# Optimization experiments

Measured on AMD Instinct MI355X. Metric: run time of the kernel, lower is better.

The kernel has to match this reference:

```python
import jax, jax.numpy as jnp
import numpy as np

TOPK = 4


def setup_inputs() -> dict:
    key = jax.random.key(0)
    ks = jax.random.split(key, 9)
    B, T, D = 4, 2048, 1024
    E, H = 32, 128          # routed experts, per-expert hidden
    HS = H * TOPK           # shared expert hidden = 512
    s = lambda k, shape, fan: jax.random.normal(k, shape, dtype=jnp.float32) / np.sqrt(fan)
    return {
        "x": jax.random.normal(ks[0], (B, T, D), dtype=jnp.float32),
        "router_w": s(ks[1], (E, D), D),
        "router_bias": jnp.zeros((E,), dtype=jnp.float32),
        "gate_w": s(ks[2], (E, H, D), D),
        "up_w": s(ks[3], (E, H, D), D),
        "down_w": s(ks[4], (E, D, H), H),
        "sgate_w": s(ks[5], (HS, D), D),
        "sup_w": s(ks[6], (HS, D), D),
        "sdown_w": s(ks[7], (D, HS), HS),
    }


def reference(x, router_w, router_bias, gate_w, up_w, down_w, sgate_w, sup_w, sdown_w):
    B, T, D = x.shape
    flat = x.reshape(B * T, D)                                   # [N, D]
    # Router (fp32 logits + persistent bias buffer)
    logits = flat.astype(jnp.float32) @ router_w.T + router_bias  # [N, E]
    scores = jax.nn.softmax(logits, axis=-1)
    topk_scores, topk_idx = jax.lax.top_k(scores, TOPK)          # [N, K]
    topk_scores = topk_scores / jnp.clip(
        topk_scores.sum(axis=-1, keepdims=True), 1e-12, None)
    # Dense all-expert SwiGLU (matches torch.stack over experts)
    h = jax.nn.silu(jnp.einsum("nd,ehd->neh", flat, gate_w)) \
        * jnp.einsum("nd,ehd->neh", flat, up_w)                  # [N, E, H]
    expert_out = jnp.einsum("neh,edh->ned", h, down_w)           # [N, E, D]
    # Gather top-k expert outputs, scale, combine
    sel = jnp.take_along_axis(expert_out, topk_idx[:, :, None], axis=1)  # [N, K, D]
    out = (sel * topk_scores.astype(flat.dtype)[:, :, None]).sum(axis=1)  # [N, D]
    # Always-on shared expert (SwiGLU)
    out = out + (jax.nn.silu(flat @ sgate_w.T) * (flat @ sup_w.T)) @ sdown_w.T
    return out.reshape(B, T, D)
```

## Files before the change

kernel.cpp:

```cpp
#include <hip/hip_runtime.h>
#include <hip/hip_bf16.h>
#include <math.h>

#define N_TOK 8192
#define DIM   1024
#define E_R   32
#define H_E   128
#define HS    512
#define TOPK  4
#define RKS   8
#define RKL   (DIM / RKS)
#define MAXSLOT 34816

typedef __bf16 bf16;
typedef __bf16 bf16x8 __attribute__((ext_vector_type(8)));
typedef float  floatx4 __attribute__((ext_vector_type(4)));

#define MFMA16(a,b,c) __builtin_amdgcn_mfma_f32_16x16x32_bf16(a,b,c,0,0,0)

__device__ __forceinline__ void gl_lds16(const bf16* g, bf16* l) {
    __builtin_amdgcn_global_load_lds(
        (const __attribute__((address_space(1))) void*)g,
        (__attribute__((address_space(3))) void*)l, 16, 0, 0);
}

__device__ __forceinline__ int xcd_swz(int b, int n) {
    int q = n >> 3, r = n & 7;
    int xcd = b & 7, idx = b >> 3;
    return (xcd < r ? xcd * (q + 1) : r * (q + 1) + (xcd - r) * q) + idx;
}

__global__ __launch_bounds__(256)
void cvt_all(const float* __restrict__ x, const float* __restrict__ g,
             const float* __restrict__ u, const float* __restrict__ d,
             const float* __restrict__ sg, const float* __restrict__ su,
             const float* __restrict__ sd,
             bf16* __restrict__ xb, bf16* __restrict__ gb, bf16* __restrict__ ub,
             bf16* __restrict__ db, bf16* __restrict__ sgb, bf16* __restrict__ sub,
             bf16* __restrict__ sdb) {
    int b = blockIdx.x;
    const float* s; bf16* o; int lb;
    if      (b < 4096)  { s = x;  o = xb;  lb = b; }
    else if (b < 6144)  { s = g;  o = gb;  lb = b - 4096; }
    else if (b < 8192)  { s = u;  o = ub;  lb = b - 6144; }
    else if (b < 10240) { s = d;  o = db;  lb = b - 8192; }
    else if (b < 10496) { s = sg; o = sgb; lb = b - 10240; }
    else if (b < 10752) { s = su; o = sub; lb = b - 10496; }
    else                { s = sd; o = sdb; lb = b - 10752; }
    size_t i = (size_t)lb * 2048 + threadIdx.x * 8;
    float4 v0 = *(const float4*)(s + i);
    float4 v1 = *(const float4*)(s + i + 4);
    bf16x8 r = {(bf16)v0.x,(bf16)v0.y,(bf16)v0.z,(bf16)v0.w,
                (bf16)v1.x,(bf16)v1.y,(bf16)v1.z,(bf16)v1.w};
    *(bf16x8*)(o + i) = r;
}

__global__ __launch_bounds__(256)
void router_gemm(const float* __restrict__ x, const float* __restrict__ rw,
                 float* __restrict__ partial) {
    __shared__ float Xs[64 * 132];
    __shared__ float Wt[128 * 32];
    int tid = threadIdx.x;
    int t0  = blockIdx.x * 64;
    int kb  = blockIdx.y * RKL;

#pragma unroll
    for (int j = 0; j < 8; ++j) {
        int flat = j * 1024 + tid * 4;
        int row = flat >> 7, col = flat & 127;
        float4 v = *(const float4*)(x + (size_t)(t0 + row) * DIM + kb + col);
        *(float4*)(&Xs[row * 132 + col]) = v;
    }
    {
        int e = tid >> 3, kq = (tid & 7) * 16;
        const float* wp = rw + (size_t)e * DIM + kb + kq;
#pragma unroll
        for (int i = 0; i < 16; i += 4) {
            float4 v = *(const float4*)(wp + i);
            Wt[(kq + i + 0) * 32 + e] = v.x;
            Wt[(kq + i + 1) * 32 + e] = v.y;
            Wt[(kq + i + 2) * 32 + e] = v.z;
            Wt[(kq + i + 3) * 32 + e] = v.w;
        }
    }
    __syncthreads();

    int eg = tid & 7, tg = tid >> 3;
    float acc[2][4] = {{0.f}};
#pragma unroll 4
    for (int k = 0; k < RKL; k += 4) {
        float4 xa0 = *(const float4*)(&Xs[(tg * 2 + 0) * 132 + k]);
        float4 xa1 = *(const float4*)(&Xs[(tg * 2 + 1) * 132 + k]);
#pragma unroll
        for (int kk = 0; kk < 4; ++kk) {
            float4 w = *(const float4*)(&Wt[(k + kk) * 32 + eg * 4]);
            float x0 = (&xa0.x)[kk], x1 = (&xa1.x)[kk];
            acc[0][0] += x0 * w.x; acc[0][1] += x0 * w.y;
            acc[0][2] += x0 * w.z; acc[0][3] += x0 * w.w;
            acc[1][0] += x1 * w.x; acc[1][1] += x1 * w.y;
            acc[1][2] += x1 * w.z; acc[1][3] += x1 * w.w;
        }
    }
#pragma unroll
    for (int t = 0; t < 2; ++t) {
        floatx4 v = { acc[t][0], acc[t][1], acc[t][2], acc[t][3] };
        *(floatx4*)(&partial[((size_t)blockIdx.y * N_TOK + t0 + tg * 2 + t) * 32 + eg * 4]) = v;
    }
}

__global__ __launch_bounds__(256)
void router_fin(const float* __restrict__ partial, const float* __restrict__ rb,
                int* __restrict__ counts, int* __restrict__ tlist,
                float* __restrict__ slist, int* __restrict__ tok2slot) {
    __shared__ int lcnt[E_R];
    __shared__ int gbase[E_R];
    int tid = threadIdx.x;
    int n = blockIdx.x * 256 + tid;
    if (tid < E_R) lcnt[tid] = 0;
    __syncthreads();

    float lg[E_R];
#pragma unroll
    for (int e4 = 0; e4 < E_R; e4 += 4) {
        floatx4 s = {0.f, 0.f, 0.f, 0.f};
#pragma unroll
        for (int ks = 0; ks < RKS; ++ks)
            s += *(const floatx4*)(&partial[((size_t)ks * N_TOK + n) * 32 + e4]);
        lg[e4 + 0] = s[0] + rb[e4 + 0];
        lg[e4 + 1] = s[1] + rb[e4 + 1];
        lg[e4 + 2] = s[2] + rb[e4 + 2];
        lg[e4 + 3] = s[3] + rb[e4 + 3];
    }
    float mx = -1e30f;
#pragma unroll
    for (int e = 0; e < E_R; ++e) mx = fmaxf(mx, lg[e]);
    float se = 0.f;
#pragma unroll
    for (int e = 0; e < E_R; ++e) { float v = __expf(lg[e] - mx); lg[e] = v; se += v; }
    float inv = 1.f / se;

    unsigned usedMask = 0;
    int idx[TOPK]; float pv[TOPK]; int lpos[TOPK]; float psum = 0.f;
    for (int k = 0; k < TOPK; ++k) {
        float best = -1.f; int bi = 0;
        for (int e = 0; e < E_R; ++e)
            if (!((usedMask >> e) & 1) && lg[e] > best) { best = lg[e]; bi = e; }
        usedMask |= 1u << bi;
        idx[k] = bi; pv[k] = best * inv; psum += pv[k];
    }
    float norm = 1.f / fmaxf(psum, 1e-12f);
#pragma unroll
    for (int k = 0; k < TOPK; ++k)
        lpos[k] = atomicAdd(&lcnt[idx[k]], 1);
    __syncthreads();
    if (tid < E_R) gbase[tid] = atomicAdd(&counts[tid], lcnt[tid]);
    __syncthreads();
#pragma unroll
    for (int k = 0; k < TOPK; ++k) {
        int e = idx[k];
        int pos = gbase[e] + lpos[k];
        tlist[(size_t)e * N_TOK + pos] = n;
        slist[(size_t)e * N_TOK + pos] = pv[k] * norm;
        tok2slot[(size_t)n * 4 + k] = (e << 16) | pos;
    }
}

__global__ void wq_build(const int* __restrict__ counts, int* __restrict__ items,
                         int* __restrict__ nitems, int* __restrict__ expbase) {
    if (threadIdx.x == 0) {
        int n = 0, base = 0;
        for (int e = 0; e < E_R; ++e) {
            int c = counts[e];
            expbase[e] = base;
            int nt = (c + 63) >> 6;
            for (int t = 0; t < nt; ++t)
                items[n++] = (e << 24) | (t << 16) | (base + t * 64);
            base += nt * 64;
        }
        *nitems = n;
    }
}

__global__ __launch_bounds__(256, 2)
void phase1(const bf16* __restrict__ xb, const bf16* __restrict__ wg,
            const bf16* __restrict__ wu, const bf16* __restrict__ sg,
            const bf16* __restrict__ su, const int* __restrict__ counts,
            const int* __restrict__ tlist, const int* __restrict__ items,
            const int* __restrict__ nitems,
            bf16* __restrict__ Hg, bf16* __restrict__ Hs) {
    __shared__ __align__(16) bf16 As[2 * 64 * 64];
    __shared__ __align__(16) bf16 Bs[2 * 256 * 64];

    int b = xcd_swz(blockIdx.x, 1056);
    const bf16 *gptr, *uptr;
    bf16* hout; int hstride;
    int e, lbase, cnt = 0;
    if (b < 512) {
        int c = b >> 7, t = b & 127;
        gptr = sg + (size_t)c * H_E * DIM;
        uptr = su + (size_t)c * H_E * DIM;
        hout = Hs + (size_t)t * 64 * HS + c * H_E;
        hstride = HS;
        lbase = t * 64;
        e = -1;
    } else {
        int rbk = b - 512;
        if (rbk >= *nitems) return;
        int it = items[rbk];
        e = it >> 24; int t = (it >> 16) & 0xff; int rowbase = it & 0xffff;
        gptr = wg + (size_t)e * H_E * DIM;
        uptr = wu + (size_t)e * H_E * DIM;
        hout = Hg + (size_t)rowbase * H_E;
        hstride = H_E;
        cnt = counts[e];
        lbase = t * 64;
    }

    int tid = threadIdx.x;
    int rs = tid >> 3;
    int cOff = ((tid & 7) ^ (rs & 7)) * 8;
    int tokA, tokB;
    if (e < 0) { tokA = lbase + rs; tokB = lbase + rs + 32; }
    else {
        int liA = lbase + rs;      if (liA >= cnt) liA = cnt - 1;
        int liB = lbase + rs + 32; if (liB >= cnt) liB = cnt - 1;
        tokA = tlist[(size_t)e * N_TOK + liA];
        tokB = tlist[(size_t)e * N_TOK + liB];
    }
    const bf16* aSrc0 = xb + (size_t)tokA * DIM + cOff;
    const bf16* aSrc1 = xb + (size_t)tokB * DIM + cOff;
    const bf16* gSrc  = gptr + (size_t)rs * DIM + cOff;
    const bf16* uSrc  = uptr + (size_t)rs * DIM + cOff;

    int w = tid >> 6, lane = tid & 63, m = lane & 15, quad = lane >> 4;
    int mx7 = m & 7;

    floatx4 aG[4][2] = {{{0}}};
    floatx4 aU[4][2] = {{{0}}};

    #define P1_STAGE(buf, k0)                                                  \
        do {                                                                   \
            bf16* aD = As + (buf) * 4096 + tid * 8;                            \
            bf16* bD = Bs + (buf) * 16384 + tid * 8;                           \
            gl_lds16(aSrc0 + (k0), aD);                                        \
            gl_lds16(aSrc1 + (k0), aD + 2048);                                 \
            gl_lds16(gSrc + (k0),            bD);                              \
            gl_lds16(gSrc + 32 * DIM + (k0), bD + 2048);                       \
            gl_lds16(gSrc + 64 * DIM + (k0), bD + 4096);                       \
            gl_lds16(gSrc + 96 * DIM + (k0), bD + 6144);                       \
            gl_lds16(uSrc + (k0),            bD + 8192);                       \
            gl_lds16(uSrc + 32 * DIM + (k0), bD + 10240);                      \
            gl_lds16(uSrc + 64 * DIM + (k0), bD + 12288);                      \
            gl_lds16(uSrc + 96 * DIM + (k0), bD + 14336);                      \
        } while (0)

    P1_STAGE(0, 0);
    __syncthreads();

    int cur = 0;
    for (int k0 = 0; k0 < DIM; k0 += 64) {
        if (k0 + 64 < DIM) P1_STAGE(cur ^ 1, k0 + 64);
        const bf16* Ab = As + cur * 4096;
        const bf16* Bb = Bs + cur * 16384;
#pragma unroll
        for (int kh = 0; kh < 2; ++kh) {
            int cx = ((kh * 4 + quad) ^ mx7) * 8;
            bf16x8 a[4], bg[2], bu[2];
#pragma unroll
            for (int mg = 0; mg < 4; ++mg)
                a[mg] = *(const bf16x8*)(Ab + (mg * 16 + m) * 64 + cx);
#pragma unroll
            for (int j = 0; j < 2; ++j) {
                bg[j] = *(const bf16x8*)(Bb + (w * 32 + j * 16 + m) * 64 + cx);
                bu[j] = *(const bf16x8*)(Bb + (128 + w * 32 + j * 16 + m) * 64 + cx);
            }
#pragma unroll
            for (int j = 0; j < 2; ++j)
#pragma unroll
                for (int mg = 0; mg < 4; ++mg) {
                    aG[mg][j] = MFMA16(a[mg], bg[j], aG[mg][j]);
                    aU[mg][j] = MFMA16(a[mg], bu[j], aU[mg][j]);
                }
        }
        __syncthreads();
        cur ^= 1;
    }
    #undef P1_STAGE

#pragma unroll
    for (int mg = 0; mg < 4; ++mg)
#pragma unroll
        for (int j = 0; j < 2; ++j)
#pragma unroll
            for (int r4 = 0; r4 < 4; ++r4) {
                float gv = aG[mg][j][r4], uv = aU[mg][j][r4];
                float h = gv / (1.f + __expf(-gv)) * uv;
                hout[(size_t)(mg * 16 + quad * 4 + r4) * hstride + w * 32 + j * 16 + m] = (bf16)h;
            }
}

__global__ __launch_bounds__(256, 4)
void phase2(const bf16* __restrict__ Hg, const bf16* __restrict__ wd,
            const int* __restrict__ counts, const float* __restrict__ slist,
            const int* __restrict__ items, const int* __restrict__ nitems,
            bf16* __restrict__ Od) {
    __shared__ __align__(16) bf16 As[2 * 64 * 32];
    __shared__ __align__(16) bf16 Bs[2 * 256 * 32];
    __shared__ float ssc[64];

    int rbk = xcd_swz(blockIdx.x, 544);
    if (rbk >= *nitems) return;
    int it = items[rbk];
    int e = it >> 24, t = (it >> 16) & 0xff, rowbase = it & 0xffff;
    int n0 = blockIdx.y * 256;
    int cnt = counts[e];

    int tid = threadIdx.x;
    if (tid < 64) {
        int li = t * 64 + tid;
        ssc[tid] = (li < cnt) ? slist[(size_t)e * N_TOK + li] : 0.f;
    }

    int r = tid >> 2;
    int chunk = (((tid & 3) ^ ((tid >> 3) & 3))) * 8;
    const bf16* aSrc = Hg + (size_t)(rowbase + r) * H_E + chunk;
    const bf16* bSrc = wd + (size_t)e * DIM * H_E + (size_t)(n0 + r) * H_E + chunk;

    int w = tid >> 6, lane = tid & 63, m = lane & 15, quad = lane >> 4;
    int quadx = quad ^ ((m >> 1) & 3);
    floatx4 acc[4][4] = {{{0}}};

    #define P2_STAGE(buf, k0)                                                  \
        do {                                                                   \
            bf16* aD = As + (buf) * 2048 + tid * 8;                            \
            bf16* bD = Bs + (buf) * 8192 + tid * 8;                            \
            gl_lds16(aSrc + (k0), aD);                                         \
            _Pragma("unroll")                                                  \
            for (int p = 0; p < 4; ++p)                                        \
                gl_lds16(bSrc + (size_t)p * 64 * H_E + (k0), bD + p * 2048);   \
        } while (0)

    P2_STAGE(0, 0);
    __syncthreads();

    int cur = 0;
    for (int k0 = 0; k0 < H_E; k0 += 32) {
        if (k0 + 32 < H_E) P2_STAGE(cur ^ 1, k0 + 32);
        const bf16* Ab = As + cur * 2048;
        const bf16* Bb = Bs + cur * 8192;
        bf16x8 a[4], bb[4];
#pragma unroll
        for (int mg = 0; mg < 4; ++mg)
            a[mg] = *(const bf16x8*)(Ab + (mg * 16 + m) * 32 + quadx * 8);
#pragma unroll
        for (int ng = 0; ng < 4; ++ng)
            bb[ng] = *(const bf16x8*)(Bb + (w * 64 + ng * 16 + m) * 32 + quadx * 8);
#pragma unroll
        for (int ng = 0; ng < 4; ++ng)
#pragma unroll
            for (int mg = 0; mg < 4; ++mg)
                acc[mg][ng] = MFMA16(a[mg], bb[ng], acc[mg][ng]);
        __syncthreads();
        cur ^= 1;
    }
    #undef P2_STAGE

#pragma unroll
    for (int mg = 0; mg < 4; ++mg)
#pragma unroll
        for (int r4 = 0; r4 < 4; ++r4) {
            int row = mg * 16 + quad * 4 + r4;
            float sc = ssc[row];
            bf16* op = Od + (size_t)(rowbase + row) * DIM + n0 + w * 64 + m;
#pragma unroll
            for (int ng = 0; ng < 4; ++ng)
                op[ng * 16] = (bf16)(acc[mg][ng][r4] * sc);
        }
}

__global__ __launch_bounds__(256, 4)
void shared_down(const bf16* __restrict__ Hs, const bf16* __restrict__ sd,
                 const bf16* __restrict__ Od, const int* __restrict__ tok2slot,
                 const int* __restrict__ expbase, float* __restrict__ out) {
    __shared__ __align__(16) bf16 As[2 * 64 * 32];
    __shared__ __align__(16) bf16 Bs[2 * 256 * 32];
    __shared__ int srow[64][4];

    int t0 = xcd_swz(blockIdx.x, 128) * 64;
    int n0 = blockIdx.y * 256;
    int tid = threadIdx.x;

    if (tid < 64) {
        const int* t2s = tok2slot + (size_t)(t0 + tid) * 4;
#pragma unroll
        for (int k = 0; k < 4; ++k) {
            int v = t2s[k];
            srow[tid][k] = expbase[v >> 16] + (v & 0xffff);
        }
    }

    int r = tid >> 2;
    int chunk = (((tid & 3) ^ ((tid >> 3) & 3))) * 8;
    const bf16* aSrc = Hs + (size_t)(t0 + r) * HS + chunk;
    const bf16* bSrc = sd + (size_t)(n0 + r) * HS + chunk;

    int w = tid >> 6, lane = tid & 63, m = lane & 15, quad = lane >> 4;
    int quadx = quad ^ ((m >> 1) & 3);
    floatx4 acc[4][4] = {{{0}}};

    #define SD_STAGE(buf, k0)                                                  \
        do {                                                                   \
            bf16* aD = As + (buf) * 2048 + tid * 8;                            \
            bf16* bD = Bs + (buf) * 8192 + tid * 8;                            \
            gl_lds16(aSrc + (k0), aD);                                         \
            _Pragma("unroll")                                                  \
            for (int p = 0; p < 4; ++p)                                        \
                gl_lds16(bSrc + (size_t)p * 64 * HS + (k0), bD + p * 2048);    \
        } while (0)

    SD_STAGE(0, 0);
    __syncthreads();

    int cur = 0;
    for (int tt = 0; tt < 16; ++tt) {
        if (tt < 15) SD_STAGE(cur ^ 1, (tt + 1) * 32);
        const bf16* Ab = As + cur * 2048;
        const bf16* Bb = Bs + cur * 8192;
        bf16x8 a[4], bb[4];
#pragma unroll
        for (int mg = 0; mg < 4; ++mg)
            a[mg] = *(const bf16x8*)(Ab + (mg * 16 + m) * 32 + quadx * 8);
#pragma unroll
        for (int ng = 0; ng < 4; ++ng)
            bb[ng] = *(const bf16x8*)(Bb + (w * 64 + ng * 16 + m) * 32 + quadx * 8);
#pragma unroll
        for (int ng = 0; ng < 4; ++ng)
#pragma unroll
            for (int mg = 0; mg < 4; ++mg)
                acc[mg][ng] = MFMA16(a[mg], bb[ng], acc[mg][ng]);
        __syncthreads();
        cur ^= 1;
    }
    #undef SD_STAGE

#pragma unroll
    for (int mg = 0; mg < 4; ++mg)
#pragma unroll
        for (int r4 = 0; r4 < 4; ++r4) {
            int rl = mg * 16 + quad * 4 + r4;
            size_t r0 = (size_t)srow[rl][0] * DIM;
            size_t r1 = (size_t)srow[rl][1] * DIM;
            size_t r2 = (size_t)srow[rl][2] * DIM;
            size_t r3 = (size_t)srow[rl][3] * DIM;
            float* op = out + (size_t)(t0 + rl) * DIM + n0 + w * 64 + m;
#pragma unroll
            for (int ng = 0; ng < 4; ++ng) {
                int col = n0 + w * 64 + ng * 16 + m;
                float v = acc[mg][ng][r4]
                        + (float)Od[r0 + col] + (float)Od[r1 + col]
                        + (float)Od[r2 + col] + (float)Od[r3 + col];
                op[ng * 16] = v;
            }
        }
}

extern "C" void kernel_launch(void* const* d_in, const int* in_sizes, int n_in,
                              void* d_out, int out_size, void* d_ws, size_t ws_size,
                              hipStream_t stream) {
    (void)in_sizes; (void)n_in; (void)out_size; (void)ws_size;
    const float* x   = (const float*)d_in[0];
    const float* rw  = (const float*)d_in[1];
    const float* rb  = (const float*)d_in[2];
    const float* gw  = (const float*)d_in[3];
    const float* uw  = (const float*)d_in[4];
    const float* dw  = (const float*)d_in[5];
    const float* sgw = (const float*)d_in[6];
    const float* suw = (const float*)d_in[7];
    const float* sdw = (const float*)d_in[8];
    float* out = (float*)d_out;

    char* ws = (char*)d_ws;
    size_t o = 0;
    bf16* xb  = (bf16*)(ws + o); o += (size_t)N_TOK * DIM * 2;
    bf16* wgb = (bf16*)(ws + o); o += (size_t)E_R * H_E * DIM * 2;
    bf16* wub = (bf16*)(ws + o); o += (size_t)E_R * H_E * DIM * 2;
    bf16* wdb = (bf16*)(ws + o); o += (size_t)E_R * DIM * H_E * 2;
    bf16* sgb = (bf16*)(ws + o); o += (size_t)HS * DIM * 2;
    bf16* sub = (bf16*)(ws + o); o += (size_t)HS * DIM * 2;
    bf16* sdb = (bf16*)(ws + o); o += (size_t)DIM * HS * 2;
    bf16* Hg  = (bf16*)(ws + o); o += (size_t)MAXSLOT * H_E * 2;
    bf16* Hs  = (bf16*)(ws + o); o += (size_t)N_TOK * HS * 2;
    bf16* Od  = (bf16*)(ws + o); o += (size_t)MAXSLOT * DIM * 2;
    float* partial = (float*)(ws + o); o += (size_t)RKS * N_TOK * 32 * 4;
    int*   counts = (int*)(ws + o);   o += 256;
    int*   tlist  = (int*)(ws + o);   o += (size_t)E_R * N_TOK * 4;
    float* slist  = (float*)(ws + o); o += (size_t)E_R * N_TOK * 4;
    int*   tok2slot = (int*)(ws + o); o += (size_t)N_TOK * 4 * 4;
    int*   items  = (int*)(ws + o);   o += 4096;
    int*   nitems = (int*)(ws + o);   o += 64;
    int*   expbase = (int*)(ws + o);  o += 256;

    hipMemsetAsync(counts, 0, E_R * sizeof(int), stream);

    router_gemm<<<dim3(N_TOK / 64, RKS), 256, 0, stream>>>(x, rw, partial);
    router_fin<<<N_TOK / 256, 256, 0, stream>>>(partial, rb, counts, tlist, slist,
                                                tok2slot);
    cvt_all<<<11008, 256, 0, stream>>>(x, gw, uw, dw, sgw, suw, sdw,
                                       xb, wgb, wub, wdb, sgb, sub, sdb);
    wq_build<<<1, 64, 0, stream>>>(counts, items, nitems, expbase);
    phase1<<<1056, 256, 0, stream>>>(xb, wgb, wub, sgb, sub, counts, tlist,
                                     items, nitems, Hg, Hs);
    phase2<<<dim3(544, 4), 256, 0, stream>>>(Hg, wdb, counts, slist,
                                             items, nitems, Od);
    shared_down<<<dim3(N_TOK / 64, 4), 256, 0, stream>>>(Hs, sdb, Od, tok2slot,
                                                         expbase, out);
}
```

Before: 292.4 us.

## Fuse routed-expert down projection into phase1 via LDS-resident hidden tile

Routed-expert blocks in phase1 now keep the SwiGLU hidden tile in LDS and run the down projection over all 1024 output columns in eight double-buffered chunks of the expert's down weights. This writes the scaled result straight to Od. The separate phase2 launch and the Hg round trip through global memory go away. In exchange, each routed block does much more serial work, and one block per tile now covers the whole output width where phase2 spread it over four blocks. That lowers parallelism for the down GEMM and may raise register pressure under launch bounds of 2.

New measurement: 313.0 us. 7.0% more time.

```diff
diff --git a/kernel.cpp b/kernel.cpp
--- a/kernel.cpp
+++ b/kernel.cpp
@@ -184,34 +184,32 @@
 __global__ __launch_bounds__(256, 2)
 void phase1(const bf16* __restrict__ xb, const bf16* __restrict__ wg,
             const bf16* __restrict__ wu, const bf16* __restrict__ sg,
-            const bf16* __restrict__ su, const int* __restrict__ counts,
-            const int* __restrict__ tlist, const int* __restrict__ items,
+            const bf16* __restrict__ su, const bf16* __restrict__ wd,
+            const int* __restrict__ counts, const int* __restrict__ tlist,
+            const float* __restrict__ slist, const int* __restrict__ items,
             const int* __restrict__ nitems,
-            bf16* __restrict__ Hg, bf16* __restrict__ Hs) {
+            bf16* __restrict__ Hs, bf16* __restrict__ Od) {
     __shared__ __align__(16) bf16 As[2 * 64 * 64];
     __shared__ __align__(16) bf16 Bs[2 * 256 * 64];
 
     int b = xcd_swz(blockIdx.x, 1056);
     const bf16 *gptr, *uptr;
-    bf16* hout; int hstride;
-    int e, lbase, cnt = 0;
+    bf16* hout = nullptr;
+    int e, lbase, cnt = 0, rowbase = 0;
     if (b < 512) {
         int c = b >> 7, t = b & 127;
         gptr = sg + (size_t)c * H_E * DIM;
         uptr = su + (size_t)c * H_E * DIM;
         hout = Hs + (size_t)t * 64 * HS + c * H_E;
-        hstride = HS;
         lbase = t * 64;
         e = -1;
     } else {
         int rbk = b - 512;
         if (rbk >= *nitems) return;
         int it = items[rbk];
-        e = it >> 24; int t = (it >> 16) & 0xff; int rowbase = it & 0xffff;
+        e = it >> 24; int t = (it >> 16) & 0xff; rowbase = it & 0xffff;
         gptr = wg + (size_t)e * H_E * DIM;
         uptr = wu + (size_t)e * H_E * DIM;
-        hout = Hg + (size_t)rowbase * H_E;
-        hstride = H_E;
         cnt = counts[e];
         lbase = t * 64;
     }
@@ -287,6 +285,21 @@
     }
     #undef P1_STAGE
 
+    if (e < 0) {
+#pragma unroll
+        for (int mg = 0; mg < 4; ++mg)
+#pragma unroll
+            for (int j = 0; j < 2; ++j)
+#pragma unroll
+                for (int r4 = 0; r4 < 4; ++r4) {
+                    float gv = aG[mg][j][r4], uv = aU[mg][j][r4];
+                    float h = gv / (1.f + __expf(-gv)) * uv;
+                    hout[(size_t)(mg * 16 + quad * 4 + r4) * HS + w * 32 + j * 16 + m] = (bf16)h;
+                }
+        return;
+    }
+
+    bf16* Ht = As;
 #pragma unroll
     for (int mg = 0; mg < 4; ++mg)
 #pragma unroll
@@ -295,87 +308,74 @@
             for (int r4 = 0; r4 < 4; ++r4) {
                 float gv = aG[mg][j][r4], uv = aU[mg][j][r4];
                 float h = gv / (1.f + __expf(-gv)) * uv;
-                hout[(size_t)(mg * 16 + quad * 4 + r4) * hstride + w * 32 + j * 16 + m] = (bf16)h;
+                int row = mg * 16 + quad * 4 + r4;
+                int col = w * 32 + j * 16 + m;
+                int cc  = col >> 3;
+                Ht[row * 128 + ((cc ^ (row & 7)) << 3) + (m & 7)] = (bf16)h;
             }
-}
-
-__global__ __launch_bounds__(256, 4)
-void phase2(const bf16* __restrict__ Hg, const bf16* __restrict__ wd,
-            const int* __restrict__ counts, const float* __restrict__ slist,
-            const int* __restrict__ items, const int* __restrict__ nitems,
-            bf16* __restrict__ Od) {
-    __shared__ __align__(16) bf16 As[2 * 64 * 32];
-    __shared__ __align__(16) bf16 Bs[2 * 256 * 32];
-    __shared__ float ssc[64];
-
-    int rbk = xcd_swz(blockIdx.x, 544);
-    if (rbk >= *nitems) return;
-    int it = items[rbk];
-    int e = it >> 24, t = (it >> 16) & 0xff, rowbase = it & 0xffff;
-    int n0 = blockIdx.y * 256;
-    int cnt = counts[e];
-
-    int tid = threadIdx.x;
-    if (tid < 64) {
-        int li = t * 64 + tid;
-        ssc[tid] = (li < cnt) ? slist[(size_t)e * N_TOK + li] : 0.f;
-    }
-
-    int r = tid >> 2;
-    int chunk = (((tid & 3) ^ ((tid >> 3) & 3))) * 8;
-    const bf16* aSrc = Hg + (size_t)(rowbase + r) * H_E + chunk;
-    const bf16* bSrc = wd + (size_t)e * DIM * H_E + (size_t)(n0 + r) * H_E + chunk;
-
-    int w = tid >> 6, lane = tid & 63, m = lane & 15, quad = lane >> 4;
-    int quadx = quad ^ ((m >> 1) & 3);
-    floatx4 acc[4][4] = {{{0}}};
-
-    #define P2_STAGE(buf, k0)                                                  \
+
+    float scv[4][4];
+#pragma unroll
+    for (int mg = 0; mg < 4; ++mg)
+#pragma unroll
+        for (int r4 = 0; r4 < 4; ++r4) {
+            int li = lbase + mg * 16 + quad * 4 + r4;
+            scv[mg][r4] = (li < cnt) ? slist[(size_t)e * N_TOK + li] : 0.f;
+        }
+
+    const bf16* wde = wd + (size_t)e * DIM * H_E;
+    int trow = tid >> 4;
+    int clog = (tid & 15) ^ (trow & 7);
+    #define DB_STAGE(half, nc)                                                 \
         do {                                                                   \
-            bf16* aD = As + (buf) * 2048 + tid * 8;                            \
-            bf16* bD = Bs + (buf) * 8192 + tid * 8;                            \
-            gl_lds16(aSrc + (k0), aD);                                         \
+            bf16* dB = Bs + (half) * 16384 + tid * 8;                          \
+            const bf16* sB = wde + ((size_t)(nc) * 128 + trow) * 128 + clog * 8; \
             _Pragma("unroll")                                                  \
-            for (int p = 0; p < 4; ++p)                                        \
-                gl_lds16(bSrc + (size_t)p * 64 * H_E + (k0), bD + p * 2048);   \
+            for (int i = 0; i < 8; ++i)                                        \
+                gl_lds16(sB + (size_t)i * 16 * 128, dB + i * 2048);            \
         } while (0)
 
-    P2_STAGE(0, 0);
-    __syncthreads();
-
-    int cur = 0;
-    for (int k0 = 0; k0 < H_E; k0 += 32) {
-        if (k0 + 32 < H_E) P2_STAGE(cur ^ 1, k0 + 32);
-        const bf16* Ab = As + cur * 2048;
-        const bf16* Bb = Bs + cur * 8192;
-        bf16x8 a[4], bb[4];
+    DB_STAGE(0, 0);
+    __syncthreads();
+
+    bf16x8 af[4][4];
+#pragma unroll
+    for (int ks = 0; ks < 4; ++ks)
 #pragma unroll
         for (int mg = 0; mg < 4; ++mg)
-            a[mg] = *(const bf16x8*)(Ab + (mg * 16 + m) * 32 + quadx * 8);
-#pragma unroll
-        for (int ng = 0; ng < 4; ++ng)
-            bb[ng] = *(const bf16x8*)(Bb + (w * 64 + ng * 16 + m) * 32 + quadx * 8);
-#pragma unroll
-        for (int ng = 0; ng < 4; ++ng)
-#pragma unroll
-            for (int mg = 0; mg < 4; ++mg)
-                acc[mg][ng] = MFMA16(a[mg], bb[ng], acc[mg][ng]);
+            af[ks][mg] = *(const bf16x8*)(Ht + (mg * 16 + m) * 128 +
+                                          ((ks * 4 + quad) ^ (m & 7)) * 8);
+
+    for (int nc = 0; nc < 8; ++nc) {
+        if (nc + 1 < 8) DB_STAGE((nc + 1) & 1, nc + 1);
+        const bf16* Bh = Bs + (nc & 1) * 16384;
+        floatx4 dacc[4][2] = {{{0}}};
+#pragma unroll
+        for (int ks = 0; ks < 4; ++ks) {
+            bf16x8 bb[2];
+#pragma unroll
+            for (int ng = 0; ng < 2; ++ng)
+                bb[ng] = *(const bf16x8*)(Bh + (w * 32 + ng * 16 + m) * 128 +
+                                          ((ks * 4 + quad) ^ (m & 7)) * 8);
+#pragma unroll
+            for (int ng = 0; ng < 2; ++ng)
+#pragma unroll
+                for (int mg = 0; mg < 4; ++mg)
+                    dacc[mg][ng] = MFMA16(af[ks][mg], bb[ng], dacc[mg][ng]);
+        }
+#pragma unroll
+        for (int mg = 0; mg < 4; ++mg)
+#pragma unroll
+            for (int r4 = 0; r4 < 4; ++r4) {
+                int row = mg * 16 + quad * 4 + r4;
+                float sc = scv[mg][r4];
+                bf16* op = Od + (size_t)(rowbase + row) * DIM + nc * 128 + w * 32 + m;
+                op[0]  = (bf16)(dacc[mg][0][r4] * sc);
+                op[16] = (bf16)(dacc[mg][1][r4] * sc);
+            }
         __syncthreads();
-        cur ^= 1;
-    }
-    #undef P2_STAGE
-
-#pragma unroll
-    for (int mg = 0; mg < 4; ++mg)
-#pragma unroll
-        for (int r4 = 0; r4 < 4; ++r4) {
-            int row = mg * 16 + quad * 4 + r4;
-            float sc = ssc[row];
-            bf16* op = Od + (size_t)(rowbase + row) * DIM + n0 + w * 64 + m;
-#pragma unroll
-            for (int ng = 0; ng < 4; ++ng)
-                op[ng * 16] = (bf16)(acc[mg][ng][r4] * sc);
-        }
+    }
+    #undef DB_STAGE
 }
 
 __global__ __launch_bounds__(256, 4)
@@ -488,7 +488,6 @@
     bf16* sgb = (bf16*)(ws + o); o += (size_t)HS * DIM * 2;
     bf16* sub = (bf16*)(ws + o); o += (size_t)HS * DIM * 2;
     bf16* sdb = (bf16*)(ws + o); o += (size_t)DIM * HS * 2;
-    bf16* Hg  = (bf16*)(ws + o); o += (size_t)MAXSLOT * H_E * 2;
     bf16* Hs  = (bf16*)(ws + o); o += (size_t)N_TOK * HS * 2;
     bf16* Od  = (bf16*)(ws + o); o += (size_t)MAXSLOT * DIM * 2;
     float* partial = (float*)(ws + o); o += (size_t)RKS * N_TOK * 32 * 4;
@@ -508,10 +507,8 @@
     cvt_all<<<11008, 256, 0, stream>>>(x, gw, uw, dw, sgw, suw, sdw,
                                        xb, wgb, wub, wdb, sgb, sub, sdb);
     wq_build<<<1, 64, 0, stream>>>(counts, items, nitems, expbase);
-    phase1<<<1056, 256, 0, stream>>>(xb, wgb, wub, sgb, sub, counts, tlist,
-                                     items, nitems, Hg, Hs);
-    phase2<<<dim3(544, 4), 256, 0, stream>>>(Hg, wdb, counts, slist,
-                                             items, nitems, Od);
+    phase1<<<1056, 256, 0, stream>>>(xb, wgb, wub, sgb, sub, wdb, counts, tlist,
+                                     slist, items, nitems, Hs, Od);
     shared_down<<<dim3(N_TOK / 64, 4), 256, 0, stream>>>(Hs, sdb, Od, tok2slot,
                                                          expbase, out);
 }
```
